# Performance work log

Hardware: AMD Instinct MI355X
Metric: run time of the kernel (lower is better)

The kernel has to match this reference:

```python
import jax, jax.numpy as jnp
import numpy as np

COMPRESS_RATE = 128
HEAD_DIM = 128
ROPE_DIM = 64
ROPE_THETA = 10000.0
EPS = 1e-6


def setup_inputs() -> dict:
    key = jax.random.key(0)
    ks = jax.random.split(key, 5)
    B, S, H = 2, 8192, 2048
    return {
        "hidden_states": jax.random.normal(ks[0], (B, S, H), jnp.float32),
        "q_residual": jax.random.normal(ks[1], (B, S, H), jnp.float32),
        "position_ids": jnp.broadcast_to(jnp.arange(S, dtype=jnp.int32), (B, S)),
        "w_kv": jax.random.normal(ks[2], (H, HEAD_DIM), jnp.float32) * 0.02,
        "w_gate": jax.random.normal(ks[3], (H, HEAD_DIM), jnp.float32) * 0.02,
        "position_bias": jax.random.normal(ks[4], (COMPRESS_RATE, HEAD_DIM), jnp.float32) * 0.02,
        "kv_norm_weight": jnp.ones((HEAD_DIM,), jnp.float32),
    }


def _rms_norm(x, w, eps=EPS):
    xf = x.astype(jnp.float32)
    var = jnp.mean(jnp.square(xf), axis=-1, keepdims=True)
    return (xf * jax.lax.rsqrt(var + eps)).astype(x.dtype) * w


def _rotate_half(x):
    x1, x2 = jnp.split(x, 2, axis=-1)
    return jnp.concatenate([-x2, x1], axis=-1)


def reference(hidden_states, q_residual, position_ids, w_kv, w_gate, position_bias, kv_norm_weight):
    # Stateless single-shot HCA compression (past_key_values is None):
    # compress every full window of COMPRESS_RATE tokens, drop the remainder.
    B, S, H = hidden_states.shape
    m, d = COMPRESS_RATE, HEAD_DIM
    T = S // m
    usable = T * m
    h = hidden_states[:, :usable]
    # eq. 20/21: C = H @ W_kv, Z = H @ W_gate
    kv = (h @ w_kv).reshape(B, T, m, d)      # [B,T,m,d]
    gate = (h @ w_gate).reshape(B, T, m, d)  # [B,T,m,d]
    # eq. 22: per-channel softmax over the window dim with position bias B
    w = jax.nn.softmax(gate + position_bias, axis=2)
    compressed = jnp.sum(w * kv, axis=2)     # [B,T,d]
    compressed = _rms_norm(compressed, kv_norm_weight)
    compressed = compressed[:, None]         # [B,1,T,d] single shared KV head
    # Interleaved RoPE at deterministic positions i * compress_rate (first_window_position = 0)
    half = ROPE_DIM // 2
    inv_freq = 1.0 / (ROPE_THETA ** (jnp.arange(half, dtype=jnp.float32) / half))
    pos = jnp.arange(T, dtype=jnp.float32) * m            # [T]
    freqs = pos[:, None] * inv_freq[None, :]              # [T, half]
    cos = jnp.repeat(jnp.cos(freqs), 2, axis=-1)[None, None]  # [1,1,T,ROPE_DIM]
    sin = jnp.repeat(jnp.sin(freqs), 2, axis=-1)[None, None]
    nope, rope = compressed[..., :-ROPE_DIM], compressed[..., -ROPE_DIM:]
    rotated = rope * cos + _rotate_half(rope) * sin
    return jnp.concatenate([nope, rotated], axis=-1)      # [B,1,T,d]
```

## Files before the change

kernel.cpp:

```cpp
#include <hip/hip_runtime.h>
#include <hip/hip_bf16.h>

#define HDIM 2048
#define DDIM 128
#define NT 256
#define BM 32
#define BK 128
#define LDK 136
#define MT 16384

typedef __attribute__((ext_vector_type(8))) short bf16x8_t;
typedef __attribute__((ext_vector_type(4))) float f32x4_t;

__global__ void k_prep(const void* __restrict__ w_kv, const void* __restrict__ w_gate,
                       const unsigned short* __restrict__ hidden,
                       int* __restrict__ flag, __hip_bfloat16* __restrict__ Wt) {
  __shared__ int sflag;
  __shared__ float tile[64][65];
  int bad = 0;
  for (int i = threadIdx.x; i < 8192; i += 256)
    bad |= (((hidden[i] >> 7) & 0xFF) >= 167) ? 1 : 0;
  if (threadIdx.x == 0) sflag = 0;
  __syncthreads();
  if (bad) atomicOr(&sflag, 1);
  __syncthreads();
  const int isF32 = sflag;
  if (threadIdx.x == 0 && blockIdx.x == 0 && blockIdx.y == 0 && blockIdx.z == 0)
    *flag = isF32;

  const void* src = blockIdx.z ? w_gate : w_kv;
  const int k0 = blockIdx.x * 64;
  const int n0 = blockIdx.y * 64;
  const int tx = threadIdx.x & 63;
  const int ty = threadIdx.x >> 6;
#pragma unroll
  for (int i = 0; i < 16; ++i) {
    int r = i * 4 + ty;
    int idx = (k0 + r) * DDIM + n0 + tx;
    float v = isF32 ? ((const float*)src)[idx]
                    : __bfloat162float(((const __hip_bfloat16*)src)[idx]);
    tile[tx][r] = v;
  }
  __syncthreads();
#pragma unroll
  for (int i = 0; i < 16; ++i) {
    int r = i * 4 + ty;
    Wt[(blockIdx.z * DDIM + n0 + r) * HDIM + k0 + tx] = __float2bfloat16(tile[r][tx]);
  }
}

__global__ __launch_bounds__(256)
void k_gemm(const void* __restrict__ hidden, const __hip_bfloat16* __restrict__ Wt,
            const int* __restrict__ flag, __hip_bfloat16* __restrict__ C) {
  __shared__ __align__(16) __hip_bfloat16 As[BM * LDK];
  const int isF32 = *flag;
  const int tid  = threadIdx.x;
  const int bm0  = blockIdx.x * BM;
  const int wave = tid >> 6;
  const int lane = tid & 63;
  const int wn   = wave * 64;
  const int lrow = lane & 15;
  const int quad = lane >> 4;

  f32x4_t acc[2][4];
#pragma unroll
  for (int i = 0; i < 2; ++i)
#pragma unroll
    for (int j = 0; j < 4; ++j) acc[i][j] = (f32x4_t){0.f, 0.f, 0.f, 0.f};

  const int srow = tid >> 3;
  const int skg  = (tid & 7) * 16;
  const float*          Af = (const float*)hidden + (size_t)(bm0 + srow) * HDIM + skg;
  const unsigned short* Ab = (const unsigned short*)hidden + (size_t)(bm0 + srow) * HDIM + skg;

  float4 pa[4];
  int4   pb[2];
  if (isF32) {
#pragma unroll
    for (int l = 0; l < 4; ++l) pa[l] = *(const float4*)(Af + 4 * l);
  } else {
#pragma unroll
    for (int l = 0; l < 2; ++l) pb[l] = *(const int4*)(Ab + 8 * l);
  }

  for (int k0 = 0; k0 < HDIM; k0 += BK) {
    __syncthreads();
    if (isF32) {
#pragma unroll
      for (int l = 0; l < 2; ++l) {
        union { int4 v; __hip_bfloat16 h[8]; } u;
        u.h[0] = __float2bfloat16(pa[2*l].x);   u.h[1] = __float2bfloat16(pa[2*l].y);
        u.h[2] = __float2bfloat16(pa[2*l].z);   u.h[3] = __float2bfloat16(pa[2*l].w);
        u.h[4] = __float2bfloat16(pa[2*l+1].x); u.h[5] = __float2bfloat16(pa[2*l+1].y);
        u.h[6] = __float2bfloat16(pa[2*l+1].z); u.h[7] = __float2bfloat16(pa[2*l+1].w);
        *(int4*)(As + srow * LDK + skg + 8 * l) = u.v;
      }
    } else {
#pragma unroll
      for (int l = 0; l < 2; ++l)
        *(int4*)(As + srow * LDK + skg + 8 * l) = pb[l];
    }
    __syncthreads();

    if (k0 + BK < HDIM) {
      if (isF32) {
#pragma unroll
        for (int l = 0; l < 4; ++l) pa[l] = *(const float4*)(Af + k0 + BK + 4 * l);
      } else {
#pragma unroll
        for (int l = 0; l < 2; ++l) pb[l] = *(const int4*)(Ab + k0 + BK + 8 * l);
      }
    }

#pragma unroll
    for (int kk = 0; kk < BK; kk += 32) {
      bf16x8_t afrag[2], bfrag[4];
#pragma unroll
      for (int nt = 0; nt < 4; ++nt)
        bfrag[nt] = *(const bf16x8_t*)(Wt + (size_t)(wn + nt * 16 + lrow) * HDIM + k0 + kk + quad * 8);
#pragma unroll
      for (int mt = 0; mt < 2; ++mt)
        afrag[mt] = *(const bf16x8_t*)(As + (mt * 16 + lrow) * LDK + kk + quad * 8);
#pragma unroll
      for (int mt = 0; mt < 2; ++mt)
#pragma unroll
        for (int nt = 0; nt < 4; ++nt)
          acc[mt][nt] = __builtin_amdgcn_mfma_f32_16x16x32_bf16(afrag[mt], bfrag[nt], acc[mt][nt], 0, 0, 0);
    }
  }

#pragma unroll
  for (int mt = 0; mt < 2; ++mt) {
    const int mrow = bm0 + mt * 16 + quad * 4;
#pragma unroll
    for (int nt = 0; nt < 4; ++nt) {
      const int ncol = wn + nt * 16 + lrow;
#pragma unroll
      for (int r = 0; r < 4; ++r)
        C[(size_t)(mrow + r) * NT + ncol] = __float2bfloat16(acc[mt][nt][r]);
    }
  }
}

__global__ __launch_bounds__(512)
void k_compress(const __hip_bfloat16* __restrict__ C,
                const void* __restrict__ pbias,
                const void* __restrict__ nw,
                const int* __restrict__ flag,
                void* __restrict__ out) {
  const int isF32 = *flag;
  const int tid = threadIdx.x;
  const int j = tid & (DDIM - 1);
  const int g = tid >> 7;
  const int bt = blockIdx.x;
  const int t  = bt & 63;
  const long i0 = (long)bt * 128;

  float mx = -3.0e38f, l = 0.f, acc = 0.f;
#pragma unroll 8
  for (int rr = 0; rr < 32; ++rr) {
    const int r = g * 32 + rr;
    const __hip_bfloat16* row = C + (i0 + r) * NT;
    float pb = isF32 ? ((const float*)pbias)[r * DDIM + j]
                     : __bfloat162float(((const __hip_bfloat16*)pbias)[r * DDIM + j]);
    float gt = __bfloat162float(row[DDIM + j]) + pb;
    float v  = __bfloat162float(row[j]);
    float nm = fmaxf(mx, gt);
    float sc = __expf(mx - nm);
    float e  = __expf(gt - nm);
    l   = l * sc + e;
    acc = acc * sc + e * v;
    mx  = nm;
  }

  __shared__ float smx[4][DDIM], sl[4][DDIM], sa[4][DDIM];
  __shared__ float sh[DDIM];
  __shared__ float ssum[2];
  smx[g][j] = mx; sl[g][j] = l; sa[g][j] = acc;
  __syncthreads();

  float comp = 0.f;
  if (g == 0) {
    float M = fmaxf(fmaxf(smx[0][j], smx[1][j]), fmaxf(smx[2][j], smx[3][j]));
    float L = 0.f, A = 0.f;
#pragma unroll
    for (int q = 0; q < 4; ++q) {
      float s = __expf(smx[q][j] - M);
      L += sl[q][j] * s;
      A += sa[q][j] * s;
    }
    comp = A / L;
    float sq = comp * comp;
#pragma unroll
    for (int off = 32; off > 0; off >>= 1) sq += __shfl_down(sq, off, 64);
    if ((j & 63) == 0) ssum[j >> 6] = sq;
  }
  __syncthreads();

  if (g == 0) {
    float var = (ssum[0] + ssum[1]) * (1.0f / DDIM);
    float wv = isF32 ? ((const float*)nw)[j] : __bfloat162float(((const __hip_bfloat16*)nw)[j]);
    float y = comp * rsqrtf(var + 1e-6f) * wv;
    sh[j] = y;
  }
  __syncthreads();

  if (g == 0) {
    float y = sh[j];
    float outv = y;
    if (j >= 64) {
      int jj = j - 64;
      int fi = jj >> 1;
      double invf = exp((double)fi * (-0.28782313662425575));
      double ang  = (double)(t * 128) * invf;
      float c = (float)cos(ang);
      float s = (float)sin(ang);
      float other = (jj < 32) ? -sh[64 + jj + 32] : sh[64 + jj - 32];
      outv = y * c + other * s;
    }
    if (isF32) ((float*)out)[bt * DDIM + j] = outv;
    else       ((__hip_bfloat16*)out)[bt * DDIM + j] = __float2bfloat16(outv);
  }
}

extern "C" void kernel_launch(void* const* d_in, const int* in_sizes, int n_in,
                              void* d_out, int out_size, void* d_ws, size_t ws_size,
                              hipStream_t stream) {
  const void* hidden = d_in[0];
  const void* w_kv   = d_in[3];
  const void* w_gate = d_in[4];
  const void* pbias  = d_in[5];
  const void* nw     = d_in[6];

  int* flag = (int*)d_ws;
  __hip_bfloat16* Wt = (__hip_bfloat16*)((char*)d_ws + 256);
  __hip_bfloat16* C  = (__hip_bfloat16*)((char*)d_ws + 256 + (size_t)NT * HDIM * sizeof(__hip_bfloat16));

  k_prep<<<dim3(HDIM / 64, DDIM / 64, 2), 256, 0, stream>>>(w_kv, w_gate,
                                                            (const unsigned short*)hidden, flag, Wt);
  k_gemm<<<dim3(MT / BM), 256, 0, stream>>>(hidden, Wt, flag, C);
  k_compress<<<dim3(128), 512, 0, stream>>>(C, pbias, nw, flag, d_out);
}
```

Measured before the change: 322.0 us.

## Split GEMM over N, stage weights in LDS via swizzled direct global-to-LDS loads

Measured after the change: 309.4 us. 1.04x faster.

```diff
diff --git a/kernel.cpp b/kernel.cpp
--- a/kernel.cpp
+++ b/kernel.cpp
@@ -5,12 +5,17 @@
 #define DDIM 128
 #define NT 256
 #define BM 32
-#define BK 128
-#define LDK 136
+#define BN 128
+#define BK 64
+#define LDA 72
 #define MT 16384
 
 typedef __attribute__((ext_vector_type(8))) short bf16x8_t;
 typedef __attribute__((ext_vector_type(4))) float f32x4_t;
+
+#define GLOAD_LDS16(gp, lp)                                                                        \
+  __builtin_amdgcn_global_load_lds((const __attribute__((address_space(1))) unsigned int*)(gp),    \
+                                   (__attribute__((address_space(3))) unsigned int*)(lp), 16, 0, 0)
 
 __global__ void k_prep(const void* __restrict__ w_kv, const void* __restrict__ w_gate,
                        const unsigned short* __restrict__ hidden,
@@ -49,83 +54,83 @@
   }
 }
 
-__global__ __launch_bounds__(256)
+__global__ __launch_bounds__(256, 4)
 void k_gemm(const void* __restrict__ hidden, const __hip_bfloat16* __restrict__ Wt,
             const int* __restrict__ flag, __hip_bfloat16* __restrict__ C) {
-  __shared__ __align__(16) __hip_bfloat16 As[BM * LDK];
+  __shared__ __align__(1024) __hip_bfloat16 Bs[BN * BK];
+  __shared__ __align__(16)   __hip_bfloat16 As[BM * LDA];
   const int isF32 = *flag;
   const int tid  = threadIdx.x;
-  const int bm0  = blockIdx.x * BM;
-  const int wave = tid >> 6;
+  const int w    = tid >> 6;
   const int lane = tid & 63;
-  const int wn   = wave * 64;
   const int lrow = lane & 15;
   const int quad = lane >> 4;
 
-  f32x4_t acc[2][4];
+  const int bw  = blockIdx.x;
+  const int L   = ((bw & 7) << 7) + (bw >> 3);
+  const int bm0 = (L >> 1) * BM;
+  const int n0  = (L & 1) * BN;
+
+  f32x4_t acc[2][2];
 #pragma unroll
   for (int i = 0; i < 2; ++i)
 #pragma unroll
-    for (int j = 0; j < 4; ++j) acc[i][j] = (f32x4_t){0.f, 0.f, 0.f, 0.f};
+    for (int j = 0; j < 2; ++j) acc[i][j] = (f32x4_t){0.f, 0.f, 0.f, 0.f};
 
   const int srow = tid >> 3;
-  const int skg  = (tid & 7) * 16;
+  const int skg  = (tid & 7) * 8;
   const float*          Af = (const float*)hidden + (size_t)(bm0 + srow) * HDIM + skg;
   const unsigned short* Ab = (const unsigned short*)hidden + (size_t)(bm0 + srow) * HDIM + skg;
 
-  float4 pa[4];
-  int4   pb[2];
-  if (isF32) {
-#pragma unroll
-    for (int l = 0; l < 4; ++l) pa[l] = *(const float4*)(Af + 4 * l);
-  } else {
-#pragma unroll
-    for (int l = 0; l < 2; ++l) pb[l] = *(const int4*)(Ab + 8 * l);
-  }
+  const int soff = (((lane & 7) ^ (lane >> 3)) << 4);
+  const char* WtB = (const char*)Wt;
+  const char* bsrc0 = WtB + (size_t)(n0 + w * 32 + 0 * 8 + (lane >> 3)) * (HDIM * 2) + soff;
+  const char* bsrc1 = WtB + (size_t)(n0 + w * 32 + 1 * 8 + (lane >> 3)) * (HDIM * 2) + soff;
+  const char* bsrc2 = WtB + (size_t)(n0 + w * 32 + 2 * 8 + (lane >> 3)) * (HDIM * 2) + soff;
+  const char* bsrc3 = WtB + (size_t)(n0 + w * 32 + 3 * 8 + (lane >> 3)) * (HDIM * 2) + soff;
+  char* ldst0 = (char*)Bs + w * 4096 + 0 * 1024;
+  char* ldst1 = (char*)Bs + w * 4096 + 1 * 1024;
+  char* ldst2 = (char*)Bs + w * 4096 + 2 * 1024;
+  char* ldst3 = (char*)Bs + w * 4096 + 3 * 1024;
+
+  float4 pa0, pa1;
+  int4   pb;
+  if (isF32) { pa0 = *(const float4*)(Af); pa1 = *(const float4*)(Af + 4); }
+  else       { pb = *(const int4*)(Ab); }
 
   for (int k0 = 0; k0 < HDIM; k0 += BK) {
     __syncthreads();
     if (isF32) {
-#pragma unroll
-      for (int l = 0; l < 2; ++l) {
-        union { int4 v; __hip_bfloat16 h[8]; } u;
-        u.h[0] = __float2bfloat16(pa[2*l].x);   u.h[1] = __float2bfloat16(pa[2*l].y);
-        u.h[2] = __float2bfloat16(pa[2*l].z);   u.h[3] = __float2bfloat16(pa[2*l].w);
-        u.h[4] = __float2bfloat16(pa[2*l+1].x); u.h[5] = __float2bfloat16(pa[2*l+1].y);
-        u.h[6] = __float2bfloat16(pa[2*l+1].z); u.h[7] = __float2bfloat16(pa[2*l+1].w);
-        *(int4*)(As + srow * LDK + skg + 8 * l) = u.v;
-      }
+      union { int4 v; __hip_bfloat16 h[8]; } u;
+      u.h[0] = __float2bfloat16(pa0.x); u.h[1] = __float2bfloat16(pa0.y);
+      u.h[2] = __float2bfloat16(pa0.z); u.h[3] = __float2bfloat16(pa0.w);
+      u.h[4] = __float2bfloat16(pa1.x); u.h[5] = __float2bfloat16(pa1.y);
+      u.h[6] = __float2bfloat16(pa1.z); u.h[7] = __float2bfloat16(pa1.w);
+      *(int4*)(As + srow * LDA + skg) = u.v;
     } else {
-#pragma unroll
-      for (int l = 0; l < 2; ++l)
-        *(int4*)(As + srow * LDK + skg + 8 * l) = pb[l];
+      *(int4*)(As + srow * LDA + skg) = pb;
+    }
+    GLOAD_LDS16(bsrc0 + 2 * k0, ldst0);
+    GLOAD_LDS16(bsrc1 + 2 * k0, ldst1);
+    GLOAD_LDS16(bsrc2 + 2 * k0, ldst2);
+    GLOAD_LDS16(bsrc3 + 2 * k0, ldst3);
+    if (k0 + BK < HDIM) {
+      if (isF32) { pa0 = *(const float4*)(Af + k0 + BK); pa1 = *(const float4*)(Af + k0 + BK + 4); }
+      else       { pb = *(const int4*)(Ab + k0 + BK); }
     }
     __syncthreads();
 
-    if (k0 + BK < HDIM) {
-      if (isF32) {
-#pragma unroll
-        for (int l = 0; l < 4; ++l) pa[l] = *(const float4*)(Af + k0 + BK + 4 * l);
-      } else {
-#pragma unroll
-        for (int l = 0; l < 2; ++l) pb[l] = *(const int4*)(Ab + k0 + BK + 8 * l);
-      }
-    }
-
-#pragma unroll
-    for (int kk = 0; kk < BK; kk += 32) {
-      bf16x8_t afrag[2], bfrag[4];
-#pragma unroll
-      for (int nt = 0; nt < 4; ++nt)
-        bfrag[nt] = *(const bf16x8_t*)(Wt + (size_t)(wn + nt * 16 + lrow) * HDIM + k0 + kk + quad * 8);
-#pragma unroll
-      for (int mt = 0; mt < 2; ++mt)
-        afrag[mt] = *(const bf16x8_t*)(As + (mt * 16 + lrow) * LDK + kk + quad * 8);
-#pragma unroll
-      for (int mt = 0; mt < 2; ++mt)
-#pragma unroll
-        for (int nt = 0; nt < 4; ++nt)
-          acc[mt][nt] = __builtin_amdgcn_mfma_f32_16x16x32_bf16(afrag[mt], bfrag[nt], acc[mt][nt], 0, 0, 0);
+#pragma unroll
+    for (int kk = 0; kk < 2; ++kk) {
+      bf16x8_t af0 = *(const bf16x8_t*)(As + (0 * 16 + lrow) * LDA + kk * 32 + quad * 8);
+      bf16x8_t af1 = *(const bf16x8_t*)(As + (1 * 16 + lrow) * LDA + kk * 32 + quad * 8);
+      const int rl0 = ((kk * 64 + quad * 16) ^ ((lrow & 7) << 4));
+      bf16x8_t bf0 = *(const bf16x8_t*)((const char*)Bs + (w * 32 + 0 * 16 + lrow) * 128 + rl0);
+      bf16x8_t bf1 = *(const bf16x8_t*)((const char*)Bs + (w * 32 + 1 * 16 + lrow) * 128 + rl0);
+      acc[0][0] = __builtin_amdgcn_mfma_f32_16x16x32_bf16(af0, bf0, acc[0][0], 0, 0, 0);
+      acc[0][1] = __builtin_amdgcn_mfma_f32_16x16x32_bf16(af0, bf1, acc[0][1], 0, 0, 0);
+      acc[1][0] = __builtin_amdgcn_mfma_f32_16x16x32_bf16(af1, bf0, acc[1][0], 0, 0, 0);
+      acc[1][1] = __builtin_amdgcn_mfma_f32_16x16x32_bf16(af1, bf1, acc[1][1], 0, 0, 0);
     }
   }
 
@@ -133,8 +138,8 @@
   for (int mt = 0; mt < 2; ++mt) {
     const int mrow = bm0 + mt * 16 + quad * 4;
 #pragma unroll
-    for (int nt = 0; nt < 4; ++nt) {
-      const int ncol = wn + nt * 16 + lrow;
+    for (int nt = 0; nt < 2; ++nt) {
+      const int ncol = n0 + w * 32 + nt * 16 + lrow;
 #pragma unroll
       for (int r = 0; r < 4; ++r)
         C[(size_t)(mrow + r) * NT + ncol] = __float2bfloat16(acc[mt][nt][r]);
@@ -238,6 +243,6 @@
 
   k_prep<<<dim3(HDIM / 64, DDIM / 64, 2), 256, 0, stream>>>(w_kv, w_gate,
                                                             (const unsigned short*)hidden, flag, Wt);
-  k_gemm<<<dim3(MT / BM), 256, 0, stream>>>(hidden, Wt, flag, C);
+  k_gemm<<<dim3((MT / BM) * 2), 256, 0, stream>>>(hidden, Wt, flag, C);
   k_compress<<<dim3(128), 512, 0, stream>>>(C, pbias, nw, flag, d_out);
 }
```
